# Optimization experiments

Measured on AMD Instinct MI355X. Metric: run time of the kernel, lower is better.

Reference implementation:

```python
import jax, jax.numpy as jnp
import numpy as np

# Model hyperparameters (match init_kwargs)
T = 3          # reasoning hops
L = 3          # rule channels (parallel LSTMs)
E = 50000      # number of entities
N = 1000000    # number of KG triples
R = 200        # r_size = (n-1)//2
NREL = 2 * R + 1  # n = 401 (forward rels, inverse rels, identity)
H = 256        # emb_size
TAU = 10.0     # tau_1 softmax temperature
TOPK = 1000    # top-k state pruning for hops t>=1
B = 8          # batch size


def setup_inputs() -> dict:
    key = jax.random.key(0)
    ks = jax.random.split(key, 16)
    s = 0.05
    return {
        "input_x": jax.random.randint(ks[0], (B,), 0, E),
        "input_r": jax.random.randint(ks[1], (B,), 0, NREL),
        "e2triple": jax.random.randint(ks[2], (3, N), 0, E),
        "triple2e": jax.random.randint(ks[3], (2, N), 0, E),
        "r2triple": jax.random.randint(ks[4], (1, N), 0, R),
        "emb": jax.random.normal(ks[5], (NREL, H), jnp.float32) * s,
        "Wih_f": jax.random.normal(ks[6], (L, 4 * H, H), jnp.float32) * s,
        "Whh_f": jax.random.normal(ks[7], (L, 4 * H, H), jnp.float32) * s,
        "bih_f": jax.random.normal(ks[8], (L, 4 * H), jnp.float32) * s,
        "bhh_f": jax.random.normal(ks[9], (L, 4 * H), jnp.float32) * s,
        "Wih_b": jax.random.normal(ks[10], (L, 4 * H, H), jnp.float32) * s,
        "Whh_b": jax.random.normal(ks[11], (L, 4 * H, H), jnp.float32) * s,
        "bih_b": jax.random.normal(ks[12], (L, 4 * H), jnp.float32) * s,
        "bhh_b": jax.random.normal(ks[13], (L, 4 * H), jnp.float32) * s,
        "linW": jax.random.normal(ks[14], (NREL, 2 * H), jnp.float32) * s,
        "linb": jax.random.normal(ks[15], (NREL,), jnp.float32) * s,
    }


def _lstm_scan(x, Wih, Whh, bih, bhh):
    # x: [S, B, H]; PyTorch gate order i, f, g, o. Returns hidden seq [S, B, H].
    Bn = x.shape[1]
    Hh = Whh.shape[1]
    pre = x @ Wih.T + bih + bhh  # hoist input projection out of the scan

    def step(carry, xt):
        h, c = carry
        g = xt + h @ Whh.T
        i, f, gg, o = jnp.split(g, 4, axis=-1)
        c = jax.nn.sigmoid(f) * c + jax.nn.sigmoid(i) * jnp.tanh(gg)
        h = jax.nn.sigmoid(o) * jnp.tanh(c)
        return (h, c), h

    init = (jnp.zeros((Bn, Hh), x.dtype), jnp.zeros((Bn, Hh), x.dtype))
    _, hs = jax.lax.scan(step, init, pre)
    return hs


def reference(input_x, input_r, e2triple, triple2e, r2triple, emb,
              Wih_f, Whh_f, bih_f, bhh_f, Wih_b, Whh_b, bih_b, bhh_b,
              linW, linb):
    Bsz = input_x.shape[0]
    x0 = jax.nn.one_hot(input_x, E, dtype=emb.dtype)  # [B, E] one-hot query entity
    q = emb[input_r]                                   # [B, H] query relation emb
    # [T+1, B, H]: T copies of the query rel emb, last step is the special emb[-1]
    seq = jnp.concatenate([
        jnp.broadcast_to(q[None], (T, Bsz, H)),
        jnp.broadcast_to(emb[-1][None, None, :], (1, Bsz, H)),
    ], axis=0)

    outs = []
    for l in range(L):  # small fixed number of structurally distinct LSTMs
        hf = _lstm_scan(seq, Wih_f[l], Whh_f[l], bih_f[l], bhh_f[l])
        hb = _lstm_scan(seq[::-1], Wih_b[l], Whh_b[l], bih_b[l], bhh_b[l])[::-1]
        rnn = jnp.concatenate([hf, hb], axis=-1).transpose(1, 0, 2)  # [B, T+1, 2H]
        outs.append(rnn[:, :-1] @ linW.T + linb)                      # [B, T, n]
    w_all = jnp.stack(outs, axis=2)  # [B, T, L, n]

    heads = e2triple[0]   # [N] head entity per triple
    tails = triple2e[1]   # [N] tail entity per triple
    tails2 = e2triple[2]  # [N] tail entity per triple (inverse-direction gather)
    rels = r2triple[0]    # [N] relation per triple, in [0, R)

    def propagate(x, w):
        # x: [B, *, E] entity state, w: [B, L, n] relation weights
        s_i = w[:, :, -1:] * x                              # identity relation
        msg_f = x[:, :, heads] * w[:, :, rels]              # [B, L, N] fwd messages
        s_h = jnp.zeros((Bsz, L, E), x.dtype).at[:, :, tails].add(msg_f)
        msg_b = x[:, :, tails2] * w[:, :, rels + R]         # inverse relations
        s_t = jnp.zeros((Bsz, L, E), x.dtype).at[:, :, heads].add(msg_b)
        return s_i + s_h + s_t

    def prune_topk(x, k):
        # keep top-k entity scores per (batch, channel), zero the rest
        th = jax.lax.top_k(x, k)[0][..., -1:]
        return jnp.where(x >= th, x, jnp.zeros((), x.dtype))

    s = None
    for t in range(T):
        w = jax.nn.softmax(w_all[:, t] / TAU, axis=-1)      # [B, L, n]
        xin = x0[:, None, :] if t == 0 else prune_topk(s, TOPK)
        st = propagate(xin, w)
        s = st / jnp.maximum(st.sum(-1, keepdims=True), 1e-7)
    return s.sum(axis=1)  # [B, E]
```

## Files before the change

### kernel.cpp

```cpp
#include <hip/hip_runtime.h>
#include <math.h>

#define TT 3
#define LL 3
#define EE 50000
#define NN 1000000
#define RR 200
#define NRELC 401
#define HH 256
#define BB 8
#define KTOP 1000
#define SROW 24
#define ROWCAP 50000

__device__ __forceinline__ float sigmoidf_(float x) {
    if (x >= 0.f) { return 1.f / (1.f + expf(-x)); }
    float z = expf(x); return z / (1.f + z);
}

__global__ __launch_bounds__(256) void pre_kernel(
    const int* __restrict__ input_r, const float* __restrict__ emb,
    const float* __restrict__ Wih_f, const float* __restrict__ bih_f, const float* __restrict__ bhh_f,
    const float* __restrict__ Wih_b, const float* __restrict__ bih_b, const float* __restrict__ bhh_b,
    float* __restrict__ preq, float* __restrict__ pree)
{
    int wave = blockIdx.x * 4 + (threadIdx.x >> 6);
    if (wave >= 1536) return;
    int lane = threadIdx.x & 63;
    int row0 = wave * 4;
    int ld = row0 >> 10;
    int l = ld >> 1, dir = ld & 1;
    const float* Wih = (dir ? Wih_b : Wih_f) + (size_t)l * 4 * HH * HH;
    const float* bih = (dir ? bih_b : bih_f) + l * 4 * HH;
    const float* bhh = (dir ? bhh_b : bhh_f) + l * 4 * HH;

    float4 xf[9];
    for (int b = 0; b < 8; ++b) {
        int r = input_r[b];
        xf[b] = *(const float4*)(emb + (size_t)r * HH + lane * 4);
    }
    xf[8] = *(const float4*)(emb + (size_t)(NRELC - 1) * HH + lane * 4);

    for (int rr = 0; rr < 4; ++rr) {
        int row = (row0 + rr) & 1023;
        float4 w4 = *(const float4*)(Wih + (size_t)row * HH + lane * 4);
        float acc[9];
        #pragma unroll
        for (int c = 0; c < 9; ++c)
            acc[c] = w4.x * xf[c].x + w4.y * xf[c].y + w4.z * xf[c].z + w4.w * xf[c].w;
        #pragma unroll
        for (int off = 32; off > 0; off >>= 1)
            #pragma unroll
            for (int c = 0; c < 9; ++c) acc[c] += __shfl_xor(acc[c], off);
        float bsum = bih[row] + bhh[row];
        if (lane < 8) preq[((size_t)ld * 8 + lane) * 1024 + row] = acc[lane] + bsum;
        if (lane == 8) pree[(size_t)ld * 1024 + row] = acc[8] + bsum;
    }
}

__global__ __launch_bounds__(256) void rec_kernel(
    const float* __restrict__ Whh_f, const float* __restrict__ Whh_b,
    const float* __restrict__ preq, const float* __restrict__ pree,
    const float* __restrict__ hstate, float* __restrict__ gates, int step)
{
    int wave = blockIdx.x * 4 + (threadIdx.x >> 6);
    if (wave >= 1536) return;
    int lane = threadIdx.x & 63;
    int row0 = wave * 4;
    int ld = row0 >> 10;
    int l = ld >> 1, dir = ld & 1;
    const float* Whh = (dir ? Whh_b : Whh_f) + (size_t)l * 4 * HH * HH;
    bool use_e = dir ? (step == 0) : (step == 3);

    float4 hf[8];
    for (int b = 0; b < 8; ++b)
        hf[b] = *(const float4*)(hstate + ((size_t)ld * 8 + b) * HH + lane * 4);

    for (int rr = 0; rr < 4; ++rr) {
        int row = (row0 + rr) & 1023;
        float4 w4 = *(const float4*)(Whh + (size_t)row * HH + lane * 4);
        float acc[8];
        #pragma unroll
        for (int b = 0; b < 8; ++b)
            acc[b] = w4.x * hf[b].x + w4.y * hf[b].y + w4.z * hf[b].z + w4.w * hf[b].w;
        #pragma unroll
        for (int off = 32; off > 0; off >>= 1)
            #pragma unroll
            for (int b = 0; b < 8; ++b) acc[b] += __shfl_xor(acc[b], off);
        if (lane < 8) {
            float pre = use_e ? pree[(size_t)ld * 1024 + row]
                              : preq[((size_t)ld * 8 + lane) * 1024 + row];
            gates[((size_t)ld * 8 + lane) * 1024 + row] = acc[lane] + pre;
        }
    }
}

__global__ __launch_bounds__(256) void hupdate_kernel(
    const float* __restrict__ preq, const float* __restrict__ pree,
    const float* __restrict__ gates, float* __restrict__ hstate,
    float* __restrict__ cstate, float* __restrict__ hbuf2, int step)
{
    int g = blockIdx.x * 256 + threadIdx.x;
    int ld = g >> 11;
    int b = (g >> 8) & 7;
    int j = g & 255;
    int dir = ld & 1;
    bool use_e = dir ? (step == 0) : (step == 3);
    float gv[4];
    #pragma unroll
    for (int q = 0; q < 4; ++q) {
        int row = q * 256 + j;
        if (step == 0)
            gv[q] = use_e ? pree[(size_t)ld * 1024 + row]
                          : preq[((size_t)ld * 8 + b) * 1024 + row];
        else
            gv[q] = gates[((size_t)ld * 8 + b) * 1024 + row];
    }
    float c = (step == 0) ? 0.f : cstate[g];
    float iv = sigmoidf_(gv[0]), fv = sigmoidf_(gv[1]);
    float gg = tanhf(gv[2]),     ov = sigmoidf_(gv[3]);
    c = fv * c + iv * gg;
    float h = ov * tanhf(c);
    cstate[g] = c;
    hstate[g] = h;
    int t_out = dir ? (3 - step) : step;
    if (t_out <= 2) hbuf2[(((size_t)ld * 8 + b) * 3 + t_out) * HH + j] = h;
}

__global__ __launch_bounds__(256) void logits_dot(
    const float* __restrict__ hbuf2, const float* __restrict__ linW,
    const float* __restrict__ linb, float* __restrict__ wbuf)
{
    int wave = blockIdx.x * 4 + (threadIdx.x >> 6);
    if (wave >= 3 * 3 * NRELC) return;
    int lane = threadIdx.x & 63;
    int n = wave % NRELC;
    int tc = wave / NRELC;
    int t = tc / 3, chunk = tc % 3;
    const float4* wr = (const float4*)(linW + (size_t)n * 2 * HH + lane * 8);
    float4 w4a = wr[0], w4b = wr[1];
    float acc[8];
    #pragma unroll
    for (int i = 0; i < 8; ++i) {
        int combo = chunk * 8 + i;
        int b = combo / 3, l = combo % 3;
        int ldh = (lane < 32) ? (l * 2 + 0) : (l * 2 + 1);
        const float* hsrc = hbuf2 + (((size_t)ldh * 8 + b) * 3 + t) * HH + (lane & 31) * 8;
        float4 f0 = *(const float4*)hsrc;
        float4 f1 = *(const float4*)(hsrc + 4);
        acc[i] = w4a.x * f0.x + w4a.y * f0.y + w4a.z * f0.z + w4a.w * f0.w
               + w4b.x * f1.x + w4b.y * f1.y + w4b.z * f1.z + w4b.w * f1.w;
    }
    #pragma unroll
    for (int off = 32; off > 0; off >>= 1)
        #pragma unroll
        for (int i = 0; i < 8; ++i) acc[i] += __shfl_xor(acc[i], off);
    if (lane < 8) {
        int combo = chunk * 8 + lane;
        wbuf[((size_t)t * 24 + combo) * NRELC + n] = acc[lane] + linb[n];
    }
}

__global__ __launch_bounds__(256) void softmax_kernel(float* __restrict__ wbuf) {
    int rowi = blockIdx.x;
    float* w = wbuf + (size_t)rowi * NRELC;
    __shared__ float red[256];
    int tid = threadIdx.x;
    float v0 = w[tid];
    float v1 = (tid + 256 < NRELC) ? w[tid + 256] : -1e30f;
    red[tid] = fmaxf(v0, v1); __syncthreads();
    for (int s2 = 128; s2 > 0; s2 >>= 1) {
        if (tid < s2) red[tid] = fmaxf(red[tid], red[tid + s2]);
        __syncthreads();
    }
    float m = red[0]; __syncthreads();
    float e0 = expf((v0 - m) * 0.1f);
    float e1 = (tid + 256 < NRELC) ? expf((v1 - m) * 0.1f) : 0.f;
    red[tid] = e0 + e1; __syncthreads();
    for (int s2 = 128; s2 > 0; s2 >>= 1) {
        if (tid < s2) red[tid] += red[tid + s2];
        __syncthreads();
    }
    float denom = red[0];
    w[tid] = e0 / denom;
    if (tid + 256 < NRELC) w[tid + 256] = e1 / denom;
}

__global__ __launch_bounds__(256) void fill_seed(
    float* __restrict__ s, const int* __restrict__ input_x, const float* __restrict__ w0,
    unsigned* __restrict__ rowcnt)
{
    __shared__ int xs[8];
    __shared__ float wv[24];
    if (threadIdx.x < 8) xs[threadIdx.x] = input_x[threadIdx.x];
    if (threadIdx.x < 24) wv[threadIdx.x] = w0[(size_t)threadIdx.x * NRELC + (NRELC - 1)];
    if (blockIdx.x == 0 && threadIdx.x < 24) rowcnt[threadIdx.x] = 0u;
    __syncthreads();
    int i = blockIdx.x * 256 + threadIdx.x;
    if (i >= SROW * EE) return;
    int row = i % 24;
    int e = i / 24;
    s[i] = (e == xs[row / 3]) ? wv[row] : 0.f;
}

__global__ __launch_bounds__(256) void hop0_scan(
    const int* __restrict__ heads, const int* __restrict__ tails,
    const int* __restrict__ tails2, const int* __restrict__ rels,
    const int* __restrict__ input_x, const float* __restrict__ w0,
    float* __restrict__ s)
{
    __shared__ int xs[BB];
    if (threadIdx.x < BB) xs[threadIdx.x] = input_x[threadIdx.x];
    __syncthreads();
    int i = blockIdx.x * 256 + threadIdx.x;
    if (i >= NN) return;
    int h = heads[i], t2 = tails2[i];
    bool any = false;
    #pragma unroll
    for (int b = 0; b < BB; ++b) any = any || (h == xs[b]) || (t2 == xs[b]);
    if (!any) return;
    int tl = tails[i], rr = rels[i];
    for (int b = 0; b < BB; ++b) {
        if (h == xs[b])
            for (int l = 0; l < LL; ++l)
                atomicAdd(&s[(size_t)tl * SROW + b * 3 + l], w0[(b * 3 + l) * NRELC + rr]);
        if (t2 == xs[b])
            for (int l = 0; l < LL; ++l)
                atomicAdd(&s[(size_t)h * SROW + b * 3 + l], w0[(b * 3 + l) * NRELC + rr + RR]);
    }
}

__global__ __launch_bounds__(256) void rowsum_compact(
    const float* __restrict__ s, float* __restrict__ partial,
    unsigned* __restrict__ ckey, unsigned* __restrict__ rowcnt, int do_compact)
{
    __shared__ float acc[24];
    __shared__ unsigned lkey[24][168];
    __shared__ unsigned lcnt[24];
    __shared__ unsigned lbase[24];
    int tid = threadIdx.x;
    if (tid < 24) { acc[tid] = 0.f; lcnt[tid] = 0u; }
    __syncthreads();
    int gidx = blockIdx.x * 256 + tid;
    int row = gidx % 24;
    float a = 0.f;
    const int total = SROW * EE;
    for (int k0 = 0; k0 < 52; k0 += 13) {
        for (int kk = 0; kk < 13; ++kk) {
            long i = (long)gidx + (long)(k0 + kk) * 24576;
            if (i < total) {
                float v = s[i];
                a += v;
                if (do_compact && __float_as_uint(v) != 0u) {
                    unsigned slot = atomicAdd(&lcnt[row], 1u);
                    slot = min(slot, 167u);
                    lkey[row][slot] = __float_as_uint(v);
                }
            }
        }
        if (do_compact) {
            __syncthreads();
            if (tid < 24) {
                unsigned c = min(lcnt[tid], 168u);
                lcnt[tid] = c;
                lbase[tid] = min(atomicAdd(&rowcnt[tid], c), (unsigned)ROWCAP);
            }
            __syncthreads();
            int r = tid % 24;
            int nthr = (r < 16) ? 11 : 10;
            unsigned cnt = lcnt[r], base = lbase[r];
            if (base + cnt > (unsigned)ROWCAP) cnt = (unsigned)ROWCAP - base;
            for (unsigned j = (unsigned)(tid / 24); j < cnt; j += nthr)
                ckey[(size_t)r * ROWCAP + base + j] = lkey[r][j];
            __syncthreads();
            if (tid < 24) lcnt[tid] = 0u;
            __syncthreads();
        }
    }
    atomicAdd(&acc[row], a);
    __syncthreads();
    if (tid < 24) partial[blockIdx.x * 24 + tid] = acc[tid];
}

__global__ __launch_bounds__(256) void rowsum_fin(
    const float* __restrict__ partial, float* __restrict__ sums,
    const float* __restrict__ w_t, float* __restrict__ wsc)
{
    int r = blockIdx.x;
    int tid = threadIdx.x;
    __shared__ float sa;
    if (tid == 0) {
        float a = 0.f;
        for (int j = 0; j < 96; ++j) a += partial[j * 24 + r];
        a = fmaxf(a, 1e-7f);
        sums[r] = a;
        sa = a;
    }
    __syncthreads();
    if (w_t != nullptr) {
        float a = sa;
        for (int i = tid; i < NRELC; i += 256)
            wsc[(size_t)r * NRELC + i] = w_t[(size_t)r * NRELC + i] / a;
    }
}

__global__ __launch_bounds__(512) void topk_select(
    const unsigned* __restrict__ ckey, const unsigned* __restrict__ rowcnt,
    float* __restrict__ th, int* __restrict__ mask)
{
    int row = blockIdx.x, tid = threadIdx.x;
    {
        int per = (EE + 23) / 24;
        int e0 = row * per, e1 = min(e0 + per, EE);
        for (int e = e0 + tid; e < e1; e += 512) mask[e] = 0;
    }
    const unsigned* keys = ckey + (size_t)row * ROWCAP;
    int n = min((int)rowcnt[row], ROWCAP);
    __shared__ unsigned hist[256];
    __shared__ int red[256];
    __shared__ int sh_bin, sh_rem;
    unsigned prefix = 0;
    int remk = KTOP;
    int iters = (n + 511) / 512;
    int lane = tid & 63;
    for (int round = 0; round < 4; ++round) {
        if (tid < 256) hist[tid] = 0u;
        __syncthreads();
        int shift = 24 - 8 * round;
        for (int it = 0; it < iters; ++it) {
            int i = it * 512 + tid;
            bool valid = (i < n);
            unsigned key = valid ? keys[i] : 0u;
            valid = valid && (round == 0 || (key >> (shift + 8)) == prefix);
            unsigned bin = valid ? ((key >> shift) & 255u) : 0u;
            unsigned long long peers = __ballot(valid);
            #pragma unroll
            for (int bit = 0; bit < 8; ++bit) {
                unsigned long long bm = __ballot(valid && ((bin >> bit) & 1u));
                peers &= ((bin >> bit) & 1u) ? bm : ~bm;
            }
            if (valid) {
                unsigned long long lower = peers & ((1ull << lane) - 1ull);
                if (lower == 0ull)
                    atomicAdd(&hist[bin], (unsigned)__popcll(peers));
            }
        }
        __syncthreads();
        if (tid < 256) red[tid] = (int)hist[tid];
        __syncthreads();
        for (int off = 1; off < 256; off <<= 1) {
            int v = 0;
            if (tid < 256 && tid + off < 256) v = red[tid + off];
            __syncthreads();
            if (tid < 256) red[tid] += v;
            __syncthreads();
        }
        if (tid == 0) { sh_bin = 0; sh_rem = remk; }
        __syncthreads();
        if (tid < 256) {
            int cnt = (int)hist[tid];
            int above = (tid == 255) ? 0 : red[tid + 1];
            if (above < remk && above + cnt >= remk) { sh_bin = tid; sh_rem = remk - above; }
        }
        __syncthreads();
        prefix = (prefix << 8) | (unsigned)sh_bin;
        remk = sh_rem;
        __syncthreads();
    }
    if (tid == 0) th[row] = __uint_as_float(prefix);
}

__global__ __launch_bounds__(256) void prune_flat(
    float* __restrict__ s, const float* __restrict__ th,
    const float* __restrict__ wsc, float* __restrict__ x, int* __restrict__ mask,
    unsigned* __restrict__ rowcnt)
{
    __shared__ float ths[24], w4s[24];
    if (threadIdx.x < 24) {
        ths[threadIdx.x] = th[threadIdx.x];
        w4s[threadIdx.x] = wsc[threadIdx.x * NRELC + (NRELC - 1)];
    }
    if (blockIdx.x == 0 && threadIdx.x < 24) rowcnt[threadIdx.x] = 0u;
    __syncthreads();
    int i = blockIdx.x * 256 + threadIdx.x;
    if (i >= SROW * EE) return;
    int row = i % 24;
    int e = i / 24;
    float v = s[i];
    float xv = (v >= ths[row]) ? v : 0.f;
    x[i] = xv;
    s[i] = w4s[row] * xv;
    if (xv > 0.f) atomicOr(&mask[e], 1 << (row / 3));
}

__global__ __launch_bounds__(256) void hop_scan(
    const int* __restrict__ heads, const int* __restrict__ tails,
    const int* __restrict__ tails2, const int* __restrict__ rels,
    const int* __restrict__ mask, const float* __restrict__ x,
    const float* __restrict__ wsc, float* __restrict__ s)
{
    int gid = blockIdx.x * 256 + threadIdx.x;
    int i = gid >> 3;
    if (i >= NN) return;
    int b = gid & 7;
    int h = heads[i], t2 = tails2[i];
    int mh = mask[h], mt = mask[t2];
    bool ah = (mh >> b) & 1;
    bool at = (mt >> b) & 1;
    if (!(ah || at)) return;
    int tl = tails[i], rr = rels[i];
    int row = b * 3;
    if (ah) {
        float v0 = x[(size_t)h * SROW + row];
        float v1 = x[(size_t)h * SROW + row + 1];
        float v2 = x[(size_t)h * SROW + row + 2];
        if (v0 != 0.f) atomicAdd(&s[(size_t)tl * SROW + row],     v0 * wsc[(row)     * NRELC + rr]);
        if (v1 != 0.f) atomicAdd(&s[(size_t)tl * SROW + row + 1], v1 * wsc[(row + 1) * NRELC + rr]);
        if (v2 != 0.f) atomicAdd(&s[(size_t)tl * SROW + row + 2], v2 * wsc[(row + 2) * NRELC + rr]);
    }
    if (at) {
        float v0 = x[(size_t)t2 * SROW + row];
        float v1 = x[(size_t)t2 * SROW + row + 1];
        float v2 = x[(size_t)t2 * SROW + row + 2];
        if (v0 != 0.f) atomicAdd(&s[(size_t)h * SROW + row],     v0 * wsc[(row)     * NRELC + rr + RR]);
        if (v1 != 0.f) atomicAdd(&s[(size_t)h * SROW + row + 1], v1 * wsc[(row + 1) * NRELC + rr + RR]);
        if (v2 != 0.f) atomicAdd(&s[(size_t)h * SROW + row + 2], v2 * wsc[(row + 2) * NRELC + rr + RR]);
    }
}

__global__ void final_kernel(const float* __restrict__ s, const float* __restrict__ sums,
                             float* __restrict__ out) {
    __shared__ float ss[24];
    if (threadIdx.x < 24) ss[threadIdx.x] = sums[threadIdx.x];
    __syncthreads();
    int e = blockIdx.x * 256 + threadIdx.x;
    if (e >= EE) return;
    const float* se = s + (size_t)e * SROW;
    #pragma unroll
    for (int b = 0; b < 8; ++b)
        out[(size_t)b * EE + e] = se[b * 3] / ss[b * 3]
                                + se[b * 3 + 1] / ss[b * 3 + 1]
                                + se[b * 3 + 2] / ss[b * 3 + 2];
}

extern "C" void kernel_launch(void* const* d_in, const int* in_sizes, int n_in,
                              void* d_out, int out_size, void* d_ws, size_t ws_size,
                              hipStream_t stream)
{
    const int*   input_x  = (const int*)d_in[0];
    const int*   input_r  = (const int*)d_in[1];
    const int*   e2triple = (const int*)d_in[2];
    const int*   triple2e = (const int*)d_in[3];
    const int*   r2triple = (const int*)d_in[4];
    const float* emb      = (const float*)d_in[5];
    const float* Wih_f    = (const float*)d_in[6];
    const float* Whh_f    = (const float*)d_in[7];
    const float* bih_f    = (const float*)d_in[8];
    const float* bhh_f    = (const float*)d_in[9];
    const float* Wih_b    = (const float*)d_in[10];
    const float* Whh_b    = (const float*)d_in[11];
    const float* bih_b    = (const float*)d_in[12];
    const float* bhh_b    = (const float*)d_in[13];
    const float* linW     = (const float*)d_in[14];
    const float* linb     = (const float*)d_in[15];

    const int* heads  = e2triple;
    const int* tails2 = e2triple + 2 * (size_t)NN;
    const int* tails  = triple2e + (size_t)NN;
    const int* rels   = r2triple;

    float* ws      = (float*)d_ws;
    float* hbuf    = ws;
    float* wbuf    = hbuf + 36864;
    float* xst     = wbuf + 28872;
    float* sst     = xst + 1200000;
    float* sums    = sst + 1200000;
    float* th      = sums + 24;
    int*   mask    = (int*)(th + 24);
    float* partial = (float*)(mask + EE);
    unsigned* rowcnt = (unsigned*)(partial + 2304);
    unsigned* ckey   = rowcnt + 32;
    float* wsc    = hbuf;
    float* preq   = xst;
    float* pree   = preq + 49152;
    float* gates  = pree + 6144;
    float* hstate = gates + 49152;
    float* cstate = hstate + 12288;

    float* out = (float*)d_out;
    const int EBLK  = (EE + 255) / 256;
    const int SBLK  = (SROW * EE + 255) / 256;
    const int NBLK  = (NN + 255) / 256;
    const int N8BLK = (NN * 8) / 256;

    pre_kernel<<<384, 256, 0, stream>>>(input_r, emb, Wih_f, bih_f, bhh_f,
                                        Wih_b, bih_b, bhh_b, preq, pree);
    hupdate_kernel<<<48, 256, 0, stream>>>(preq, pree, gates, hstate, cstate, hbuf, 0);
    for (int s = 1; s <= 3; ++s) {
        rec_kernel<<<384, 256, 0, stream>>>(Whh_f, Whh_b, preq, pree, hstate, gates, s);
        hupdate_kernel<<<48, 256, 0, stream>>>(preq, pree, gates, hstate, cstate, hbuf, s);
    }
    logits_dot<<<903, 256, 0, stream>>>(hbuf, linW, linb, wbuf);
    softmax_kernel<<<72, 256, 0, stream>>>(wbuf);

    fill_seed<<<SBLK, 256, 0, stream>>>(sst, input_x, wbuf, rowcnt);
    hop0_scan<<<NBLK, 256, 0, stream>>>(heads, tails, tails2, rels, input_x, wbuf, sst);
    rowsum_compact<<<96, 256, 0, stream>>>(sst, partial, ckey, rowcnt, 1);
    rowsum_fin<<<24, 256, 0, stream>>>(partial, sums, wbuf + 1 * 24 * NRELC, wsc);

    for (int t = 1; t < TT; ++t) {
        topk_select<<<24, 512, 0, stream>>>(ckey, rowcnt, th, mask);
        prune_flat<<<SBLK, 256, 0, stream>>>(sst, th, wsc, xst, mask, rowcnt);
        hop_scan<<<N8BLK, 256, 0, stream>>>(heads, tails, tails2, rels, mask, xst, wsc, sst);
        rowsum_compact<<<96, 256, 0, stream>>>(sst, partial, ckey, rowcnt,
                                               (t + 1 < TT) ? 1 : 0);
        const float* w_next = (t + 1 < TT) ? (wbuf + (size_t)(t + 1) * 24 * NRELC) : nullptr;
        rowsum_fin<<<24, 256, 0, stream>>>(partial, sums, w_next, wsc);
    }

    final_kernel<<<EBLK, 256, 0, stream>>>(sst, sums, out);
}
```

Baseline: 359.0 us.

## Compact active triple-batch pairs into a worklist before hop propagation

The hop kernel used to launch one thread per (triple, batch) pair, 8M threads, and most of them exit after reading the mask. A new pass now reads the mask once per triple, prefix-scans the active batch bits within each block, and appends packed (triple, batch, direction) entries to a global worklist through one atomic per block. A grid-stride kernel then handles only the listed entries. This adds an extra launch, one global atomic per block and worklist traffic in exchange for less idle work. The worklist reuses the ckey buffer, and its counter sits in the rowcnt slot that prune_flat now also resets.

```diff
diff --git a/kernel.cpp b/kernel.cpp
--- a/kernel.cpp
+++ b/kernel.cpp
@@ -12,6 +12,7 @@
 #define KTOP 1000
 #define SROW 24
 #define ROWCAP 50000
+#define WLCAP (SROW * EE)
 
 __device__ __forceinline__ float sigmoidf_(float x) {
     if (x >= 0.f) { return 1.f / (1.f + expf(-x)); }
@@ -380,7 +381,7 @@
         ths[threadIdx.x] = th[threadIdx.x];
         w4s[threadIdx.x] = wsc[threadIdx.x * NRELC + (NRELC - 1)];
     }
-    if (blockIdx.x == 0 && threadIdx.x < 24) rowcnt[threadIdx.x] = 0u;
+    if (blockIdx.x == 0 && threadIdx.x < 25) rowcnt[threadIdx.x] = 0u;
     __syncthreads();
     int i = blockIdx.x * 256 + threadIdx.x;
     if (i >= SROW * EE) return;
@@ -393,38 +394,77 @@
     if (xv > 0.f) atomicOr(&mask[e], 1 << (row / 3));
 }
 
-__global__ __launch_bounds__(256) void hop_scan(
+__global__ __launch_bounds__(256) void build_wl(
+    const int* __restrict__ heads, const int* __restrict__ tails2,
+    const int* __restrict__ mask, unsigned* __restrict__ wl,
+    unsigned* __restrict__ wlcnt)
+{
+    int tid = threadIdx.x;
+    int i = blockIdx.x * 256 + tid;
+    unsigned mh = 0, mt = 0;
+    if (i < NN) {
+        mh = (unsigned)mask[heads[i]] & 255u;
+        mt = (unsigned)mask[tails2[i]] & 255u;
+    }
+    unsigned act = mh | mt;
+    int cnt = __popc(act);
+    __shared__ int sc[256];
+    __shared__ unsigned base_s;
+    sc[tid] = cnt; __syncthreads();
+    #pragma unroll
+    for (int off = 1; off < 256; off <<= 1) {
+        int v = (tid >= off) ? sc[tid - off] : 0;
+        __syncthreads();
+        sc[tid] += v;
+        __syncthreads();
+    }
+    if (tid == 255) base_s = atomicAdd(wlcnt, (unsigned)sc[255]);
+    __syncthreads();
+    unsigned p = base_s + (unsigned)(sc[tid] - cnt);
+    while (act) {
+        int b = __ffs(act) - 1; act &= act - 1;
+        unsigned e = ((unsigned)i << 5) | ((unsigned)b << 2)
+                   | (((mh >> b) & 1u) << 1) | ((mt >> b) & 1u);
+        if (p < (unsigned)WLCAP) wl[p] = e;
+        ++p;
+    }
+}
+
+__global__ __launch_bounds__(256) void hop_work(
     const int* __restrict__ heads, const int* __restrict__ tails,
     const int* __restrict__ tails2, const int* __restrict__ rels,
-    const int* __restrict__ mask, const float* __restrict__ x,
-    const float* __restrict__ wsc, float* __restrict__ s)
-{
-    int gid = blockIdx.x * 256 + threadIdx.x;
-    int i = gid >> 3;
-    if (i >= NN) return;
-    int b = gid & 7;
-    int h = heads[i], t2 = tails2[i];
-    int mh = mask[h], mt = mask[t2];
-    bool ah = (mh >> b) & 1;
-    bool at = (mt >> b) & 1;
-    if (!(ah || at)) return;
-    int tl = tails[i], rr = rels[i];
-    int row = b * 3;
-    if (ah) {
-        float v0 = x[(size_t)h * SROW + row];
-        float v1 = x[(size_t)h * SROW + row + 1];
-        float v2 = x[(size_t)h * SROW + row + 2];
-        if (v0 != 0.f) atomicAdd(&s[(size_t)tl * SROW + row],     v0 * wsc[(row)     * NRELC + rr]);
-        if (v1 != 0.f) atomicAdd(&s[(size_t)tl * SROW + row + 1], v1 * wsc[(row + 1) * NRELC + rr]);
-        if (v2 != 0.f) atomicAdd(&s[(size_t)tl * SROW + row + 2], v2 * wsc[(row + 2) * NRELC + rr]);
-    }
-    if (at) {
-        float v0 = x[(size_t)t2 * SROW + row];
-        float v1 = x[(size_t)t2 * SROW + row + 1];
-        float v2 = x[(size_t)t2 * SROW + row + 2];
-        if (v0 != 0.f) atomicAdd(&s[(size_t)h * SROW + row],     v0 * wsc[(row)     * NRELC + rr + RR]);
-        if (v1 != 0.f) atomicAdd(&s[(size_t)h * SROW + row + 1], v1 * wsc[(row + 1) * NRELC + rr + RR]);
-        if (v2 != 0.f) atomicAdd(&s[(size_t)h * SROW + row + 2], v2 * wsc[(row + 2) * NRELC + rr + RR]);
+    const unsigned* __restrict__ wl, const unsigned* __restrict__ wlcnt,
+    const float* __restrict__ x, const float* __restrict__ wsc,
+    float* __restrict__ s)
+{
+    unsigned n = min(*wlcnt, (unsigned)WLCAP);
+    for (unsigned j = blockIdx.x * 256 + threadIdx.x; j < n; j += gridDim.x * 256) {
+        unsigned e = wl[j];
+        int i = (int)(e >> 5);
+        int b = (int)((e >> 2) & 7u);
+        bool ah = (e >> 1) & 1u;
+        bool at = e & 1u;
+        int rr = rels[i];
+        int h = heads[i];
+        int row = b * 3;
+        if (ah) {
+            int tl = tails[i];
+            float v0 = x[(size_t)h * SROW + row];
+            float v1 = x[(size_t)h * SROW + row + 1];
+            float v2 = x[(size_t)h * SROW + row + 2];
+            if (v0 != 0.f) atomicAdd(&s[(size_t)tl * SROW + row],     v0 * wsc[(row)     * NRELC + rr]);
+            if (v1 != 0.f) atomicAdd(&s[(size_t)tl * SROW + row + 1], v1 * wsc[(row + 1) * NRELC + rr]);
+            if (v2 != 0.f) atomicAdd(&s[(size_t)tl * SROW + row + 2], v2 * wsc[(row + 2) * NRELC + rr]);
+        }
+        if (at) {
+            int t2 = tails2[i];
+            float v0 = x[(size_t)t2 * SROW + row];
+            float v1 = x[(size_t)t2 * SROW + row + 1];
+            float v2 = x[(size_t)t2 * SROW + row + 2];
+            if (v0 != 0.f) atomicAdd(&s[(size_t)h * SROW + row],     v0 * wsc[(row)     * NRELC + rr + RR]);
+            if (v1 != 0.f) atomicAdd(&s[(size_t)h * SROW + row + 1], v1 * wsc[(row + 1) * NRELC + rr + RR]);
+            if (v2 != 0.f) atomicAdd(&s[(size_t)h * SROW + row + 2], v2 * wsc[(row + 2) * NRELC + rr + RR]);
+        }
     }
 }
 
@@ -486,12 +526,13 @@
     float* gates  = pree + 6144;
     float* hstate = gates + 49152;
     float* cstate = hstate + 12288;
+    unsigned* wl    = ckey;
+    unsigned* wlcnt = rowcnt + 24;
 
     float* out = (float*)d_out;
     const int EBLK  = (EE + 255) / 256;
     const int SBLK  = (SROW * EE + 255) / 256;
     const int NBLK  = (NN + 255) / 256;
-    const int N8BLK = (NN * 8) / 256;
 
     pre_kernel<<<384, 256, 0, stream>>>(input_r, emb, Wih_f, bih_f, bhh_f,
                                         Wih_b, bih_b, bhh_b, preq, pree);
@@ -511,7 +552,9 @@
     for (int t = 1; t < TT; ++t) {
         topk_select<<<24, 512, 0, stream>>>(ckey, rowcnt, th, mask);
         prune_flat<<<SBLK, 256, 0, stream>>>(sst, th, wsc, xst, mask, rowcnt);
-        hop_scan<<<N8BLK, 256, 0, stream>>>(heads, tails, tails2, rels, mask, xst, wsc, sst);
+        build_wl<<<NBLK, 256, 0, stream>>>(heads, tails2, mask, wl, wlcnt);
+        hop_work<<<1024, 256, 0, stream>>>(heads, tails, tails2, rels, wl, wlcnt,
+                                           xst, wsc, sst);
         rowsum_compact<<<96, 256, 0, stream>>>(sst, partial, ckey, rowcnt,
                                                (t + 1 < TT) ? 1 : 0);
         const float* w_next = (t + 1 < TT) ? (wbuf + (size_t)(t + 1) * 24 * NRELC) : nullptr;
```

Result: slower. 427.5 us (+19.1%).

## Build destination-sorted CSR per call and replace atomic hop scatter with gather

Applied to the files above, without the earlier changes.

Each call now builds a CSR adjacency grouped by destination entity (count, three-pass prefix scan, fill) for both forward and inverse edges. For hops t>=1 it swaps the per-triple atomic scatter for a per-(entity, batch) gather that accumulates in registers and does one plain write. This removes atomic contention and the scan over all triples times batch. In exchange it adds six CSR-build kernels with atomics on every call, and the gather threads have uneven degree-dependent work and scattered loads. The path only runs when the workspace is large enough.

```diff
diff --git a/kernel.cpp b/kernel.cpp
--- a/kernel.cpp
+++ b/kernel.cpp
@@ -12,6 +12,7 @@
 #define KTOP 1000
 #define SROW 24
 #define ROWCAP 50000
+#define NSEG (2 * EE)
 
 __device__ __forceinline__ float sigmoidf_(float x) {
     if (x >= 0.f) { return 1.f / (1.f + expf(-x)); }
@@ -428,6 +429,127 @@
     }
 }
 
+__global__ __launch_bounds__(256) void zero_u(unsigned* __restrict__ p, int n) {
+    int i = blockIdx.x * 256 + threadIdx.x;
+    if (i < n) p[i] = 0u;
+}
+
+__global__ __launch_bounds__(256) void csr_count(
+    const int* __restrict__ heads, const int* __restrict__ tails,
+    unsigned* __restrict__ off)
+{
+    int i = blockIdx.x * 256 + threadIdx.x;
+    if (i >= NN) return;
+    atomicAdd(&off[tails[i]], 1u);
+    atomicAdd(&off[EE + heads[i]], 1u);
+}
+
+__global__ __launch_bounds__(256) void csr_scan1(
+    unsigned* __restrict__ off, unsigned* __restrict__ spart)
+{
+    __shared__ unsigned sc[256];
+    int tid = threadIdx.x;
+    int idx = blockIdx.x * 256 + tid;
+    unsigned v = (idx < NSEG) ? off[idx] : 0u;
+    sc[tid] = v; __syncthreads();
+    #pragma unroll
+    for (int o = 1; o < 256; o <<= 1) {
+        unsigned u = (tid >= o) ? sc[tid - o] : 0u;
+        __syncthreads();
+        sc[tid] += u;
+        __syncthreads();
+    }
+    if (idx < NSEG) off[idx] = sc[tid] - v;
+    if (tid == 255) spart[blockIdx.x] = sc[255];
+}
+
+__global__ __launch_bounds__(512) void csr_scan2(unsigned* __restrict__ spart, int nblk) {
+    __shared__ unsigned sc[512];
+    int tid = threadIdx.x;
+    unsigned v = (tid < nblk) ? spart[tid] : 0u;
+    sc[tid] = v; __syncthreads();
+    #pragma unroll
+    for (int o = 1; o < 512; o <<= 1) {
+        unsigned u = (tid >= o) ? sc[tid - o] : 0u;
+        __syncthreads();
+        sc[tid] += u;
+        __syncthreads();
+    }
+    if (tid < nblk) spart[tid] = sc[tid] - v;
+}
+
+__global__ __launch_bounds__(256) void csr_scan3(
+    unsigned* __restrict__ off, const unsigned* __restrict__ spart,
+    unsigned* __restrict__ cur)
+{
+    int idx = blockIdx.x * 256 + threadIdx.x;
+    if (idx < NSEG) {
+        off[idx] += spart[blockIdx.x];
+        cur[idx] = 0u;
+    }
+    if (idx == 0) off[NSEG] = 2u * NN;
+}
+
+__global__ __launch_bounds__(256) void csr_fill(
+    const int* __restrict__ heads, const int* __restrict__ tails,
+    const int* __restrict__ tails2, const int* __restrict__ rels,
+    const unsigned* __restrict__ off, unsigned* __restrict__ cur,
+    unsigned* __restrict__ csr)
+{
+    int i = blockIdx.x * 256 + threadIdx.x;
+    if (i >= NN) return;
+    unsigned rl = (unsigned)rels[i];
+    int d = tails[i];
+    unsigned slot = off[d] + atomicAdd(&cur[d], 1u);
+    csr[slot] = ((unsigned)heads[i] << 8) | rl;
+    int d2 = EE + heads[i];
+    unsigned slot2 = off[d2] + atomicAdd(&cur[d2], 1u);
+    csr[slot2] = ((unsigned)tails2[i] << 8) | rl;
+}
+
+__global__ __launch_bounds__(256) void hop_gather(
+    const unsigned* __restrict__ off, const unsigned* __restrict__ csr,
+    const int* __restrict__ mask, const float* __restrict__ x,
+    const float* __restrict__ wsc, float* __restrict__ s)
+{
+    int u = blockIdx.x * 256 + threadIdx.x;
+    if (u >= EE * 8) return;
+    int e = u >> 3, b = u & 7, row = b * 3;
+    unsigned f0 = off[e], f1 = off[e + 1];
+    unsigned g0 = off[EE + e], g1 = off[EE + e + 1];
+    if (f0 == f1 && g0 == g1) return;
+    float a0 = 0.f, a1 = 0.f, a2 = 0.f;
+    const float* wr0 = wsc + (size_t)row * NRELC;
+    const float* wr1 = wr0 + NRELC;
+    const float* wr2 = wr1 + NRELC;
+    for (unsigned j = f0; j < f1; ++j) {
+        unsigned p = csr[j];
+        int src = (int)(p >> 8);
+        if ((mask[src] >> b) & 1) {
+            int rl = (int)(p & 255u);
+            const float* xs = x + (size_t)src * SROW + row;
+            a0 += xs[0] * wr0[rl];
+            a1 += xs[1] * wr1[rl];
+            a2 += xs[2] * wr2[rl];
+        }
+    }
+    for (unsigned j = g0; j < g1; ++j) {
+        unsigned p = csr[j];
+        int src = (int)(p >> 8);
+        if ((mask[src] >> b) & 1) {
+            int rl = (int)(p & 255u) + RR;
+            const float* xs = x + (size_t)src * SROW + row;
+            a0 += xs[0] * wr0[rl];
+            a1 += xs[1] * wr1[rl];
+            a2 += xs[2] * wr2[rl];
+        }
+    }
+    if (a0 != 0.f || a1 != 0.f || a2 != 0.f) {
+        float* sp = s + (size_t)e * SROW + row;
+        sp[0] += a0; sp[1] += a1; sp[2] += a2;
+    }
+}
+
 __global__ void final_kernel(const float* __restrict__ s, const float* __restrict__ sums,
                              float* __restrict__ out) {
     __shared__ float ss[24];
@@ -480,6 +602,12 @@
     float* partial = (float*)(mask + EE);
     unsigned* rowcnt = (unsigned*)(partial + 2304);
     unsigned* ckey   = rowcnt + 32;
+    unsigned* off  = ckey + 1200000;
+    unsigned* cur  = off + (NSEG + 1);
+    unsigned* spart = cur + NSEG;
+    unsigned* csr  = spart + 512;
+    const size_t NEED_CSR = (size_t)(3718120 + (NSEG + 1) + NSEG + 512 + 2 * NN) * 4;
+    const bool use_csr = (ws_size >= NEED_CSR);
     float* wsc    = hbuf;
     float* preq   = xst;
     float* pree   = preq + 49152;
@@ -492,6 +620,8 @@
     const int SBLK  = (SROW * EE + 255) / 256;
     const int NBLK  = (NN + 255) / 256;
     const int N8BLK = (NN * 8) / 256;
+    const int SEGBLK = (NSEG + 255) / 256;
+    const int GBLK  = (EE * 8 + 255) / 256;
 
     pre_kernel<<<384, 256, 0, stream>>>(input_r, emb, Wih_f, bih_f, bhh_f,
                                         Wih_b, bih_b, bhh_b, preq, pree);
@@ -503,6 +633,15 @@
     logits_dot<<<903, 256, 0, stream>>>(hbuf, linW, linb, wbuf);
     softmax_kernel<<<72, 256, 0, stream>>>(wbuf);
 
+    if (use_csr) {
+        zero_u<<<SEGBLK, 256, 0, stream>>>(off, NSEG + 1);
+        csr_count<<<NBLK, 256, 0, stream>>>(heads, tails, off);
+        csr_scan1<<<SEGBLK, 256, 0, stream>>>(off, spart);
+        csr_scan2<<<1, 512, 0, stream>>>(spart, SEGBLK);
+        csr_scan3<<<SEGBLK, 256, 0, stream>>>(off, spart, cur);
+        csr_fill<<<NBLK, 256, 0, stream>>>(heads, tails, tails2, rels, off, cur, csr);
+    }
+
     fill_seed<<<SBLK, 256, 0, stream>>>(sst, input_x, wbuf, rowcnt);
     hop0_scan<<<NBLK, 256, 0, stream>>>(heads, tails, tails2, rels, input_x, wbuf, sst);
     rowsum_compact<<<96, 256, 0, stream>>>(sst, partial, ckey, rowcnt, 1);
@@ -511,7 +650,10 @@
     for (int t = 1; t < TT; ++t) {
         topk_select<<<24, 512, 0, stream>>>(ckey, rowcnt, th, mask);
         prune_flat<<<SBLK, 256, 0, stream>>>(sst, th, wsc, xst, mask, rowcnt);
-        hop_scan<<<N8BLK, 256, 0, stream>>>(heads, tails, tails2, rels, mask, xst, wsc, sst);
+        if (use_csr)
+            hop_gather<<<GBLK, 256, 0, stream>>>(off, csr, mask, xst, wsc, sst);
+        else
+            hop_scan<<<N8BLK, 256, 0, stream>>>(heads, tails, tails2, rels, mask, xst, wsc, sst);
         rowsum_compact<<<96, 256, 0, stream>>>(sst, partial, ckey, rowcnt,
                                                (t + 1 < TT) ? 1 : 0);
         const float* w_next = (t + 1 < TT) ? (wbuf + (size_t)(t + 1) * 24 * NRELC) : nullptr;
```

Result: slower. 556.9 us (+55.1%).

## Build destination-sorted CSR of triples and replace atomic scatter with gather

Applied to the files above, without the earlier changes.

Adds a per-call two-level bucket sort that builds a CSR of incoming edges per destination entity, packing local destination, source and relation into 32-bit words. Hops 1 and 2 then use a gather kernel where 8 lanes per entity accumulate 24 channels in registers, with relation weights transposed into shared memory, instead of scanning all triples and doing atomics. The aim is to remove atomic contention and scattered writes, at the cost of building the CSR on every call (several passes over the 1M triples) and uneven per-entity work. It only runs if the workspace is large enough; otherwise it falls back to the old scan.

```diff
diff --git a/kernel.cpp b/kernel.cpp
--- a/kernel.cpp
+++ b/kernel.cpp
@@ -12,6 +12,9 @@
 #define KTOP 1000
 #define SROW 24
 #define ROWCAP 50000
+#define NBUCK 391
+#define BSH 7
+#define CSRN (2 * NN)
 
 __device__ __forceinline__ float sigmoidf_(float x) {
     if (x >= 0.f) { return 1.f / (1.f + expf(-x)); }
@@ -428,6 +431,150 @@
     }
 }
 
+__global__ __launch_bounds__(256) void zero_u(unsigned* __restrict__ p, int n) {
+    int i = blockIdx.x * 256 + threadIdx.x;
+    if (i < n) p[i] = 0u;
+}
+
+__global__ __launch_bounds__(256) void csr_count0(
+    const int* __restrict__ heads, const int* __restrict__ tails,
+    unsigned* __restrict__ gcnt)
+{
+    __shared__ unsigned h[NBUCK];
+    int tid = threadIdx.x;
+    for (int i = tid; i < NBUCK; i += 256) h[i] = 0u;
+    __syncthreads();
+    int i = blockIdx.x * 256 + tid;
+    if (i < NN) {
+        atomicAdd(&h[tails[i] >> BSH], 1u);
+        atomicAdd(&h[heads[i] >> BSH], 1u);
+    }
+    __syncthreads();
+    for (int j = tid; j < NBUCK; j += 256)
+        if (h[j]) atomicAdd(&gcnt[j], h[j]);
+}
+
+__global__ __launch_bounds__(512) void csr_scan(
+    const unsigned* __restrict__ gcnt, unsigned* __restrict__ gOff,
+    unsigned* __restrict__ gcur, unsigned* __restrict__ off)
+{
+    __shared__ unsigned sc[512];
+    int tid = threadIdx.x;
+    unsigned v = (tid < NBUCK) ? gcnt[tid] : 0u;
+    sc[tid] = v; __syncthreads();
+    #pragma unroll
+    for (int o = 1; o < 512; o <<= 1) {
+        unsigned u = (tid >= o) ? sc[tid - o] : 0u;
+        __syncthreads();
+        sc[tid] += u;
+        __syncthreads();
+    }
+    if (tid < NBUCK) { unsigned ex = sc[tid] - v; gOff[tid] = ex; gcur[tid] = ex; }
+    if (tid == NBUCK - 1) gOff[NBUCK] = sc[tid];
+    if (tid == 0) off[EE] = (unsigned)CSRN;
+}
+
+__global__ __launch_bounds__(256) void csr_stage(
+    const int* __restrict__ heads, const int* __restrict__ tails,
+    const int* __restrict__ tails2, const int* __restrict__ rels,
+    unsigned* __restrict__ gcur, unsigned* __restrict__ staging)
+{
+    int i = blockIdx.x * 256 + threadIdx.x;
+    if (i >= NN) return;
+    unsigned rl = (unsigned)rels[i];
+    int d1 = tails[i];
+    unsigned e1 = ((unsigned)(d1 & 127) << 25) | ((unsigned)heads[i] << 9) | rl;
+    unsigned p1 = atomicAdd(&gcur[d1 >> BSH], 1u);
+    if (p1 < (unsigned)CSRN) staging[p1] = e1;
+    int d2 = heads[i];
+    unsigned e2 = ((unsigned)(d2 & 127) << 25) | ((unsigned)tails2[i] << 9) | (rl + RR);
+    unsigned p2 = atomicAdd(&gcur[d2 >> BSH], 1u);
+    if (p2 < (unsigned)CSRN) staging[p2] = e2;
+}
+
+__global__ __launch_bounds__(256) void csr_bucket(
+    const unsigned* __restrict__ gOff, const unsigned* __restrict__ staging,
+    unsigned* __restrict__ off, unsigned* __restrict__ csr)
+{
+    int bk = blockIdx.x, tid = threadIdx.x;
+    unsigned base = gOff[bk], end = gOff[bk + 1];
+    __shared__ unsigned hist[128], sc[128], cur[128];
+    if (tid < 128) { hist[tid] = 0u; cur[tid] = 0u; }
+    __syncthreads();
+    for (unsigned j = base + tid; j < end; j += 256)
+        atomicAdd(&hist[staging[j] >> 25], 1u);
+    __syncthreads();
+    if (tid < 128) sc[tid] = hist[tid];
+    __syncthreads();
+    for (int o = 1; o < 128; o <<= 1) {
+        unsigned v = 0;
+        if (tid < 128 && tid >= o) v = sc[tid - o];
+        __syncthreads();
+        if (tid < 128) sc[tid] += v;
+        __syncthreads();
+    }
+    if (tid < 128) {
+        int e = bk * 128 + tid;
+        if (e < EE) off[e] = base + sc[tid] - hist[tid];
+    }
+    __syncthreads();
+    for (unsigned j = base + tid; j < end; j += 256) {
+        unsigned v = staging[j];
+        unsigned dl = v >> 25;
+        unsigned pos = base + sc[dl] - hist[dl] + atomicAdd(&cur[dl], 1u);
+        if (pos < (unsigned)CSRN) csr[pos] = v & 0x1FFFFFFu;
+    }
+}
+
+__global__ __launch_bounds__(256) void hop_gather2(
+    const unsigned* __restrict__ off, const unsigned* __restrict__ csr,
+    const int* __restrict__ mask, const float* __restrict__ x,
+    const float* __restrict__ wsc, float* __restrict__ s)
+{
+    __shared__ float wT[400 * 24];
+    for (int i = threadIdx.x; i < 400 * 24; i += 256) {
+        int rel = i / 24, row = i % 24;
+        wT[i] = wsc[(size_t)row * NRELC + rel];
+    }
+    __syncthreads();
+    int u = blockIdx.x * 256 + threadIdx.x;
+    int e = u >> 3, k = u & 7;
+    if (e >= EE) return;
+    unsigned j0 = off[e], j1 = off[e + 1];
+    float acc[24];
+    #pragma unroll
+    for (int c = 0; c < 24; ++c) acc[c] = 0.f;
+    for (unsigned j = j0 + k; j < j1; j += 8) {
+        unsigned p = csr[j];
+        int src = (int)(p >> 9);
+        int m = mask[src];
+        if (!m) continue;
+        int rel = (int)(p & 511u);
+        const float* xs = x + (size_t)src * SROW;
+        const float* wr = wT + rel * 24;
+        #pragma unroll
+        for (int b = 0; b < 8; ++b) {
+            if ((m >> b) & 1) {
+                int r = b * 3;
+                acc[r]     += xs[r]     * wr[r];
+                acc[r + 1] += xs[r + 1] * wr[r + 1];
+                acc[r + 2] += xs[r + 2] * wr[r + 2];
+            }
+        }
+    }
+    #pragma unroll
+    for (int c = 0; c < 24; ++c) {
+        acc[c] += __shfl_xor(acc[c], 1);
+        acc[c] += __shfl_xor(acc[c], 2);
+        acc[c] += __shfl_xor(acc[c], 4);
+    }
+    if (k == 0) {
+        float* sp = s + (size_t)e * SROW;
+        #pragma unroll
+        for (int c = 0; c < 24; ++c) sp[c] += acc[c];
+    }
+}
+
 __global__ void final_kernel(const float* __restrict__ s, const float* __restrict__ sums,
                              float* __restrict__ out) {
     __shared__ float ss[24];
@@ -480,6 +627,14 @@
     float* partial = (float*)(mask + EE);
     unsigned* rowcnt = (unsigned*)(partial + 2304);
     unsigned* ckey   = rowcnt + 32;
+    unsigned* off  = ckey + 1200000;
+    unsigned* gcnt = off + 50004;
+    unsigned* gOff = gcnt + 392;
+    unsigned* gcur = gOff + 392;
+    unsigned* csr  = gcur + 392;
+    unsigned* staging = (unsigned*)xst;
+    const size_t NEED_CSR = (size_t)(3718120 + 50004 + 3 * 392 + CSRN) * 4;
+    const bool use_csr = (ws_size >= NEED_CSR);
     float* wsc    = hbuf;
     float* preq   = xst;
     float* pree   = preq + 49152;
@@ -492,6 +647,7 @@
     const int SBLK  = (SROW * EE + 255) / 256;
     const int NBLK  = (NN + 255) / 256;
     const int N8BLK = (NN * 8) / 256;
+    const int GBLK2 = (EE * 8 + 255) / 256;
 
     pre_kernel<<<384, 256, 0, stream>>>(input_r, emb, Wih_f, bih_f, bhh_f,
                                         Wih_b, bih_b, bhh_b, preq, pree);
@@ -503,6 +659,14 @@
     logits_dot<<<903, 256, 0, stream>>>(hbuf, linW, linb, wbuf);
     softmax_kernel<<<72, 256, 0, stream>>>(wbuf);
 
+    if (use_csr) {
+        zero_u<<<2, 256, 0, stream>>>(gcnt, NBUCK);
+        csr_count0<<<NBLK, 256, 0, stream>>>(heads, tails, gcnt);
+        csr_scan<<<1, 512, 0, stream>>>(gcnt, gOff, gcur, off);
+        csr_stage<<<NBLK, 256, 0, stream>>>(heads, tails, tails2, rels, gcur, staging);
+        csr_bucket<<<NBUCK, 256, 0, stream>>>(gOff, staging, off, csr);
+    }
+
     fill_seed<<<SBLK, 256, 0, stream>>>(sst, input_x, wbuf, rowcnt);
     hop0_scan<<<NBLK, 256, 0, stream>>>(heads, tails, tails2, rels, input_x, wbuf, sst);
     rowsum_compact<<<96, 256, 0, stream>>>(sst, partial, ckey, rowcnt, 1);
@@ -511,7 +675,10 @@
     for (int t = 1; t < TT; ++t) {
         topk_select<<<24, 512, 0, stream>>>(ckey, rowcnt, th, mask);
         prune_flat<<<SBLK, 256, 0, stream>>>(sst, th, wsc, xst, mask, rowcnt);
-        hop_scan<<<N8BLK, 256, 0, stream>>>(heads, tails, tails2, rels, mask, xst, wsc, sst);
+        if (use_csr)
+            hop_gather2<<<GBLK2, 256, 0, stream>>>(off, csr, mask, xst, wsc, sst);
+        else
+            hop_scan<<<N8BLK, 256, 0, stream>>>(heads, tails, tails2, rels, mask, xst, wsc, sst);
         rowsum_compact<<<96, 256, 0, stream>>>(sst, partial, ckey, rowcnt,
                                                (t + 1 < TT) ? 1 : 0);
         const float* w_next = (t + 1 < TT) ? (wbuf + (size_t)(t + 1) * 24 * NRELC) : nullptr;
```

Result: slower. 1.231 ms (+242.9%).
